# Kernel tuning notes

Measured on AMD Instinct MI355X. Metric: run time of the kernel, lower is better.

The kernel has to match this reference:

```python
import jax, jax.numpy as jnp
import numpy as np
from jax import lax


def avg_pool3(x):
    # F.avg_pool2d(x, 3, 1, 1) with count_include_pad=True: zero-pad, divide by 9.
    s = lax.reduce_window(x, 0.0, lax.add, (1, 1, 3, 3), (1, 1, 1, 1),
                          [(0, 0), (0, 0), (1, 1), (1, 1)])
    return s / 9.0


def resize_bilinear_ac(x, H, W):
    # bilinear resize with align_corners=True, separable gathers
    B, C, h, w = x.shape
    if (h, w) == (H, W):
        return x
    yc = jnp.linspace(0.0, h - 1.0, H)
    xc = jnp.linspace(0.0, w - 1.0, W)
    y0 = jnp.floor(yc).astype(jnp.int32); y1 = jnp.minimum(y0 + 1, h - 1)
    x0 = jnp.floor(xc).astype(jnp.int32); x1 = jnp.minimum(x0 + 1, w - 1)
    wy = (yc - y0).astype(x.dtype)
    wx = (xc - x0).astype(x.dtype)
    xr = x[:, :, y0, :] * (1.0 - wy)[None, None, :, None] + x[:, :, y1, :] * wy[None, None, :, None]
    return xr[:, :, :, x0] * (1.0 - wx) + xr[:, :, :, x1] * wx


def grid_sample_border(img, grid):
    # F.grid_sample(mode='bilinear', padding_mode='border', align_corners=True)
    B, C, H, W = img.shape
    x = jnp.clip((grid[..., 0] + 1.0) * 0.5 * (W - 1), 0.0, W - 1.0)
    y = jnp.clip((grid[..., 1] + 1.0) * 0.5 * (H - 1), 0.0, H - 1.0)
    x0 = jnp.floor(x).astype(jnp.int32); y0 = jnp.floor(y).astype(jnp.int32)
    x1 = jnp.minimum(x0 + 1, W - 1); y1 = jnp.minimum(y0 + 1, H - 1)
    wx = (x - x0)[..., None]; wy = (y - y0)[..., None]
    imt = jnp.transpose(img, (0, 2, 3, 1))  # [B,H,W,C]
    b = jnp.arange(B)[:, None, None]
    v00 = imt[b, y0, x0]; v01 = imt[b, y0, x1]
    v10 = imt[b, y1, x0]; v11 = imt[b, y1, x1]
    top = v00 * (1.0 - wx) + v01 * wx
    bot = v10 * (1.0 - wx) + v11 * wx
    out = top * (1.0 - wy) + bot * wy
    return jnp.transpose(out, (0, 3, 1, 2))


def warp_image(img, flow):
    B, C, H, W = img.shape
    _, _, h, w = flow.shape
    flow = resize_bilinear_ac(flow, H, W)
    scale = jnp.array([W / w, H / h], dtype=img.dtype).reshape(1, 2, 1, 1)
    flow = flow * scale
    yy, xx = jnp.meshgrid(jnp.linspace(-1.0, 1.0, H, dtype=img.dtype),
                          jnp.linspace(-1.0, 1.0, W, dtype=img.dtype), indexing='ij')
    base = jnp.stack((xx, yy), axis=-1)[None]  # [1,H,W,2]
    fn = jnp.stack([2.0 * flow[:, 0] / max(W - 1, 1),
                    2.0 * flow[:, 1] / max(H - 1, 1)], axis=-1)  # [B,H,W,2]
    return grid_sample_border(img, base + fn)


def ssim_map(x, y, C1=0.01 ** 2, C2=0.03 ** 2):
    mu_x = avg_pool3(x); mu_y = avg_pool3(y)
    sigma_x = avg_pool3(x * x) - mu_x * mu_x
    sigma_y = avg_pool3(y * y) - mu_y * mu_y
    sigma_xy = avg_pool3(x * y) - mu_x * mu_y
    ssim = (2 * mu_x * mu_y + C1) * (2 * sigma_xy + C2) / \
           ((mu_x ** 2 + mu_y ** 2 + C1) * (sigma_x + sigma_y + C2) + 1e-12)
    return jnp.mean(jnp.clip((1.0 - ssim) / 2.0, 0.0, 1.0), axis=1, keepdims=True)


def masked_mean(x, mask):
    m = (mask > 0.5).astype(x.dtype)
    num = jnp.sum(x * m)
    den = jnp.maximum(jnp.sum(m), 1.0)
    return num / den


def smoothness_loss(flow):
    dx = jnp.abs(flow[:, :, :, :-1] - flow[:, :, :, 1:])
    dy = jnp.abs(flow[:, :, :-1, :] - flow[:, :, 1:, :])
    return jnp.mean(dx) + jnp.mean(dy)


def setup_inputs() -> dict:
    key = jax.random.key(0)
    k1, k2, k3, k4 = jax.random.split(key, 4)
    B, H, W = 8, 512, 1024
    h, w = 128, 256
    return {
        'flow': jax.random.normal(k1, (B, 2, h, w), dtype=jnp.float32),
        'img1': jax.random.uniform(k2, (B, 3, H, W), dtype=jnp.float32),
        'img2': jax.random.uniform(k3, (B, 3, H, W), dtype=jnp.float32),
        'valid_mask': jax.random.uniform(k4, (B, 1, H, W), dtype=jnp.float32),
    }


def reference(flow, img1, img2, valid_mask):
    alpha_photo, alpha_smooth = 1.0, 0.1
    img2_warp = warp_image(img2, flow)
    l1 = jnp.mean(jnp.abs(img1 - img2_warp), axis=1, keepdims=True)
    photo_map = 0.85 * ssim_map(img1, img2_warp) + 0.15 * l1
    photo = masked_mean(photo_map, valid_mask)
    smooth = smoothness_loss(flow)
    total = alpha_photo * photo + alpha_smooth * smooth
    return (total, photo, smooth)
```

## Files before the change

kernel.cpp:

```cpp
#include <hip/hip_runtime.h>
#include <hip/hip_fp16.h>

#define B_   8
#define H_   512
#define W_   1024
#define FH_  128
#define FW_  256
#define TW   64
#define TH   16
#define HW_  (TW + 2)
#define HH_  (TH + 2)
#define NHALO (HH_ * HW_)
#define FR_  8
#define FC_  20
#define NSLOT 256
#define PLANE (H_ * W_)

struct alignas(8) H4 { __half2 a; __half2 b; };

__device__ __forceinline__ float wave_reduce(float v) {
    #pragma unroll
    for (int off = 32; off > 0; off >>= 1) v += __shfl_down(v, off, 64);
    return v;
}

__device__ __forceinline__ void hrow(const __half2* __restrict__ s,
                                     float& hA, float& hB, float& hAA, float& hBB, float& hAB) {
    const float2 p0 = __half22float2(s[0]);
    const float2 p1 = __half22float2(s[1]);
    const float2 p2 = __half22float2(s[2]);
    hA  = p0.x + p1.x + p2.x;
    hB  = p0.y + p1.y + p2.y;
    hAA = fmaf(p0.x, p0.x, fmaf(p1.x, p1.x, p2.x * p2.x));
    hBB = fmaf(p0.y, p0.y, fmaf(p1.y, p1.y, p2.y * p2.y));
    hAB = fmaf(p0.x, p0.y, fmaf(p1.x, p1.y, p2.x * p2.y));
}

__global__ __launch_bounds__(256)
void pack_img2(const float* __restrict__ img2, H4* __restrict__ pk) {
    const int total = B_ * PLANE;
    const int stride = gridDim.x * 256 * 4;
    for (int base = (blockIdx.x * 256 + threadIdx.x) * 4; base < total; base += stride) {
        const int b = base >> 19;
        const int p = base & (PLANE - 1);
        const float* pr = img2 + (size_t)b * 3 * PLANE;
        const float4 r  = *(const float4*)&pr[p];
        const float4 g  = *(const float4*)&pr[p + PLANE];
        const float4 bl = *(const float4*)&pr[p + 2 * PLANE];
        H4* o = pk + (size_t)b * PLANE + p;
        o[0] = { __floats2half2_rn(r.x, g.x), __floats2half2_rn(bl.x, 0.f) };
        o[1] = { __floats2half2_rn(r.y, g.y), __floats2half2_rn(bl.y, 0.f) };
        o[2] = { __floats2half2_rn(r.z, g.z), __floats2half2_rn(bl.z, 0.f) };
        o[3] = { __floats2half2_rn(r.w, g.w), __floats2half2_rn(bl.w, 0.f) };
    }
}

template <int PK>
__global__ __launch_bounds__(256, 8)
void fused_main(const float* __restrict__ flow, const float* __restrict__ img1,
                const float* __restrict__ img2, const float* __restrict__ mask,
                const H4* __restrict__ pk, float* __restrict__ accum) {
    const int bid = blockIdx.x;
    const int lin = (bid & 7) * 512 + (bid >> 3);
    const int b   = lin >> 9;
    const int rem = lin & 511;
    const int ty0 = (rem >> 4) * TH;
    const int tx0 = (rem & 15) * TW;
    const int tid = threadIdx.x;

    __shared__ __half2 sP[3][HH_][HW_];
    __shared__ float   sF[2][FR_][FC_];

    const float* f0  = flow + (size_t)b * 2 * FH_ * FW_;
    const float* f1  = f0 + FH_ * FW_;
    const float* i10 = img1 + (size_t)b * 3 * PLANE;
    const float* i11 = i10 + PLANE;
    const float* i12 = i11 + PLANE;
    const float* i20 = img2 + (size_t)b * 3 * PLANE;
    const float* i21 = i20 + PLANE;
    const float* i22 = i21 + PLANE;
    const H4*    pkb = pk + (size_t)b * PLANE;

    const int fx0s = (tx0 > 0) ? (int)((float)(tx0 - 1) * (255.0f / 1023.0f)) : 0;
    const int fy0s = (ty0 > 0) ? (int)((float)(ty0 - 1) * (127.0f / 511.0f)) : 0;
    for (int i = tid; i < 2 * FR_ * FC_; i += 256) {
        const int ch = i / (FR_ * FC_);
        const int r  = (i - ch * FR_ * FC_) / FC_;
        const int cc = i - ch * FR_ * FC_ - r * FC_;
        const int sy = min(fy0s + r, FH_ - 1);
        const int sx = min(fx0s + cc, FW_ - 1);
        const float* fp = ch ? f1 : f0;
        sF[ch][r][cc] = fp[(uint32_t)sy * FW_ + (uint32_t)sx];
    }

    const int lx  = tid & 63;
    const int lyg = tid >> 6;
    const int rb  = lyg * 4;
    const float* mb = mask + (size_t)b * PLANE;
    const uint32_t mb0 = (uint32_t)(ty0 + rb) * W_ + (uint32_t)(tx0 + lx);
    float mreg[4];
    #pragma unroll
    for (int k = 0; k < 4; ++k) mreg[k] = mb[mb0 + (uint32_t)k * W_];

    __syncthreads();

    for (int i = tid; i < NHALO; i += 256) {
        const int ly = i / HW_;
        const int lxh = i - ly * HW_;
        const int gy = ty0 + ly - 1;
        const int gx = tx0 + lxh - 1;
        float v10 = 0.f, v11 = 0.f, v12 = 0.f;
        float v20 = 0.f, v21 = 0.f, v22 = 0.f;
        if (gy >= 0 && gy < H_ && gx >= 0 && gx < W_) {
            const uint32_t p = (uint32_t)gy * W_ + (uint32_t)gx;
            v10 = i10[p]; v11 = i11[p]; v12 = i12[p];

            const float yc = gy * (127.0f / 511.0f);
            const float xc = gx * (255.0f / 1023.0f);
            const int y0 = (int)yc, x0 = (int)xc;
            const float wy = yc - (float)y0, wx = xc - (float)x0;
            const int yr = y0 - fy0s, xr = x0 - fx0s;
            const float a00 = sF[0][yr][xr],     a01 = sF[0][yr][xr + 1];
            const float a10 = sF[0][yr + 1][xr], a11 = sF[0][yr + 1][xr + 1];
            const float c00 = sF[1][yr][xr],     c01 = sF[1][yr][xr + 1];
            const float c10 = sF[1][yr + 1][xr], c11 = sF[1][yr + 1][xr + 1];
            const float fxt = fmaf(wx, a01 - a00, a00);
            const float fxb = fmaf(wx, a11 - a10, a10);
            const float fx  = fmaf(wy, fxb - fxt, fxt);
            const float fyt = fmaf(wx, c01 - c00, c00);
            const float fyb = fmaf(wx, c11 - c10, c10);
            const float fy  = fmaf(wy, fyb - fyt, fyt);

            const float gxs = fminf(fmaxf(fmaf(4.0f, fx, (float)gx), 0.0f), (float)(W_ - 1));
            const float gys = fminf(fmaxf(fmaf(4.0f, fy, (float)gy), 0.0f), (float)(H_ - 1));
            const int sx0 = (int)gxs, sy0 = (int)gys;
            const int sx1 = min(sx0 + 1, W_ - 1);
            const int sy1 = min(sy0 + 1, H_ - 1);
            const float swx = gxs - (float)sx0, swy = gys - (float)sy0;
            const uint32_t p00 = (uint32_t)sy0 * W_ + (uint32_t)sx0;
            const uint32_t p01 = (uint32_t)sy0 * W_ + (uint32_t)sx1;
            const uint32_t p10 = (uint32_t)sy1 * W_ + (uint32_t)sx0;
            const uint32_t p11 = (uint32_t)sy1 * W_ + (uint32_t)sx1;

            if (PK) {
                const H4 q00 = pkb[p00], q01 = pkb[p01], q10 = pkb[p10], q11 = pkb[p11];
                const float2 rg00 = __half22float2(q00.a), rg01 = __half22float2(q01.a);
                const float2 rg10 = __half22float2(q10.a), rg11 = __half22float2(q11.a);
                const float b00 = __low2float(q00.b), b01 = __low2float(q01.b);
                const float b10 = __low2float(q10.b), b11 = __low2float(q11.b);
                {
                    const float t = fmaf(swx, rg01.x - rg00.x, rg00.x);
                    const float u = fmaf(swx, rg11.x - rg10.x, rg10.x);
                    v20 = fmaf(swy, u - t, t);
                }
                {
                    const float t = fmaf(swx, rg01.y - rg00.y, rg00.y);
                    const float u = fmaf(swx, rg11.y - rg10.y, rg10.y);
                    v21 = fmaf(swy, u - t, t);
                }
                {
                    const float t = fmaf(swx, b01 - b00, b00);
                    const float u = fmaf(swx, b11 - b10, b10);
                    v22 = fmaf(swy, u - t, t);
                }
            } else {
                {
                    const float t = fmaf(swx, i20[p01] - i20[p00], i20[p00]);
                    const float u = fmaf(swx, i20[p11] - i20[p10], i20[p10]);
                    v20 = fmaf(swy, u - t, t);
                }
                {
                    const float t = fmaf(swx, i21[p01] - i21[p00], i21[p00]);
                    const float u = fmaf(swx, i21[p11] - i21[p10], i21[p10]);
                    v21 = fmaf(swy, u - t, t);
                }
                {
                    const float t = fmaf(swx, i22[p01] - i22[p00], i22[p00]);
                    const float u = fmaf(swx, i22[p11] - i22[p10], i22[p10]);
                    v22 = fmaf(swy, u - t, t);
                }
            }
        }
        sP[0][ly][lxh] = __floats2half2_rn(v10, v20);
        sP[1][ly][lxh] = __floats2half2_rn(v11, v21);
        sP[2][ly][lxh] = __floats2half2_rn(v12, v22);
    }

    __syncthreads();

    const float inv9 = 1.0f / 9.0f;
    const float C1 = 0.0001f, C2 = 0.0009f;
    float dist[4] = {0.f, 0.f, 0.f, 0.f};
    float l1s [4] = {0.f, 0.f, 0.f, 0.f};

    #pragma unroll
    for (int c = 0; c < 3; ++c) {
        float hA0,hB0,hAA0,hBB0,hAB0;
        float hA1,hB1,hAA1,hBB1,hAB1;
        float hA2,hB2,hAA2,hBB2,hAB2;
        hrow(&sP[c][rb + 0][lx], hA0,hB0,hAA0,hBB0,hAB0);
        hrow(&sP[c][rb + 1][lx], hA1,hB1,hAA1,hBB1,hAB1);
        #pragma unroll
        for (int k = 0; k < 4; ++k) {
            hrow(&sP[c][rb + k + 2][lx], hA2,hB2,hAA2,hBB2,hAB2);
            const float sA  = hA0  + hA1  + hA2;
            const float sB  = hB0  + hB1  + hB2;
            const float sAA = hAA0 + hAA1 + hAA2;
            const float sBB = hBB0 + hBB1 + hBB2;
            const float sAB = hAB0 + hAB1 + hAB2;
            const float mx  = sA * inv9, my = sB * inv9;
            const float vx  = fmaf(-mx, mx, sAA * inv9);
            const float vy  = fmaf(-my, my, sBB * inv9);
            const float vxy = fmaf(-mx, my, sAB * inv9);
            const float numt = (2.f * mx * my + C1) * (2.f * vxy + C2);
            const float dent = fmaf(fmaf(mx, mx, fmaf(my, my, C1)), (vx + vy + C2), 1e-12f);
            const float ssim = numt * __builtin_amdgcn_rcpf(dent);
            dist[k] += fminf(fmaxf((1.0f - ssim) * 0.5f, 0.f), 1.f);
            const float2 ctr = __half22float2(sP[c][rb + k + 1][lx + 1]);
            l1s[k] += fabsf(ctr.x - ctr.y);
            hA0 = hA1; hB0 = hB1; hAA0 = hAA1; hBB0 = hBB1; hAB0 = hAB1;
            hA1 = hA2; hB1 = hB2; hAA1 = hAA2; hBB1 = hBB2; hAB1 = hAB2;
        }
    }

    float num_acc = 0.f, den_acc = 0.f;
    #pragma unroll
    for (int k = 0; k < 4; ++k) {
        const float pmv = 0.28333334f * dist[k] + 0.05f * l1s[k];
        const float m   = (mreg[k] > 0.5f) ? 1.f : 0.f;
        num_acc = fmaf(pmv, m, num_acc);
        den_acc += m;
    }

    float num = wave_reduce(num_acc);
    float den = wave_reduce(den_acc);
    __shared__ float rn[4], rd[4];
    const int wid = tid >> 6, lane = tid & 63;
    if (lane == 0) { rn[wid] = num; rd[wid] = den; }
    __syncthreads();
    if (tid == 0) {
        float* slot = accum + (size_t)(bid & (NSLOT - 1)) * 4;
        atomicAdd(&slot[0], rn[0] + rn[1] + rn[2] + rn[3]);
        atomicAdd(&slot[1], rd[0] + rd[1] + rd[2] + rd[3]);
    }
}

__global__ __launch_bounds__(256)
void smooth_kernel(const float* __restrict__ flow, float* __restrict__ accum) {
    const int N = B_ * 2 * FH_ * FW_;
    float dxs = 0.f, dys = 0.f;
    for (int i = blockIdx.x * 256 + threadIdx.x; i < N; i += gridDim.x * 256) {
        const float f = flow[i];
        const int x = i & (FW_ - 1);
        const int y = (i >> 8) & (FH_ - 1);
        if (x < FW_ - 1) dxs += fabsf(f - flow[i + 1]);
        if (y < FH_ - 1) dys += fabsf(f - flow[i + FW_]);
    }
    dxs = wave_reduce(dxs);
    dys = wave_reduce(dys);
    __shared__ float rn[4], rd[4];
    const int wid = threadIdx.x >> 6, lane = threadIdx.x & 63;
    if (lane == 0) { rn[wid] = dxs; rd[wid] = dys; }
    __syncthreads();
    if (threadIdx.x == 0) {
        float* slot = accum + (size_t)blockIdx.x * 4;
        atomicAdd(&slot[2], rn[0] + rn[1] + rn[2] + rn[3]);
        atomicAdd(&slot[3], rd[0] + rd[1] + rd[2] + rd[3]);
    }
}

__global__ __launch_bounds__(256)
void finalize_kernel(const float* __restrict__ accum, float* __restrict__ out) {
    const int t = threadIdx.x;
    float num = accum[t * 4 + 0];
    float den = accum[t * 4 + 1];
    float dxs = accum[t * 4 + 2];
    float dys = accum[t * 4 + 3];
    num = wave_reduce(num); den = wave_reduce(den);
    dxs = wave_reduce(dxs); dys = wave_reduce(dys);
    __shared__ float r[4][4];
    const int wid = t >> 6, lane = t & 63;
    if (lane == 0) { r[wid][0] = num; r[wid][1] = den; r[wid][2] = dxs; r[wid][3] = dys; }
    __syncthreads();
    if (t == 0) {
        const float tn = r[0][0] + r[1][0] + r[2][0] + r[3][0];
        const float td = r[0][1] + r[1][1] + r[2][1] + r[3][1];
        const float tx = r[0][2] + r[1][2] + r[2][2] + r[3][2];
        const float ty = r[0][3] + r[1][3] + r[2][3] + r[3][3];
        const float photo   = tn / fmaxf(td, 1.0f);
        const float mean_dx = tx / (float)(B_ * 2 * FH_ * (FW_ - 1));
        const float mean_dy = ty / (float)(B_ * 2 * (FH_ - 1) * FW_);
        const float smooth  = mean_dx + mean_dy;
        out[0] = photo + 0.1f * smooth;
        out[1] = photo;
        out[2] = smooth;
    }
}

extern "C" void kernel_launch(void* const* d_in, const int* in_sizes, int n_in,
                              void* d_out, int out_size, void* d_ws, size_t ws_size,
                              hipStream_t stream) {
    const float* flow = (const float*)d_in[0];
    const float* img1 = (const float*)d_in[1];
    const float* img2 = (const float*)d_in[2];
    const float* mask = (const float*)d_in[3];
    float* out   = (float*)d_out;
    float* accum = (float*)d_ws;
    H4*    pk    = (H4*)((char*)d_ws + 4096);

    const size_t need = 4096 + sizeof(H4) * (size_t)B_ * PLANE;
    const bool packed = ws_size >= need;

    hipMemsetAsync(accum, 0, NSLOT * 4 * sizeof(float), stream);
    smooth_kernel<<<NSLOT, 256, 0, stream>>>(flow, accum);
    const int grid = (W_ / TW) * (H_ / TH) * B_;
    if (packed) {
        pack_img2<<<2048, 256, 0, stream>>>(img2, pk);
        fused_main<1><<<grid, 256, 0, stream>>>(flow, img1, img2, mask, pk, accum);
    } else {
        fused_main<0><<<grid, 256, 0, stream>>>(flow, img1, img2, mask, pk, accum);
    }
    finalize_kernel<<<1, 256, 0, stream>>>(accum, out);
}
```

Measured before the change: 187.9 us.

## Materialize warped img2 in separate kernel and compute SSIM window sums in packed half

Replaces the pack-to-half prepass with a kernel that computes the bilinear-warped img2 once per pixel, gathering from fp32 img2, and stores it as packed half. The main kernel then reads the precomputed warp for its halo tile, which removes the redundant warp computation on halo pixels and the shared flow staging. Separately, the 3x3 window sums, squares and cross products are computed with packed half2 arithmetic instead of fp32 to cut ALU work. This risks precision loss in variance terms and adds a full-image write/read round trip through the workspace.

```diff
diff --git a/kernel.cpp b/kernel.cpp
--- a/kernel.cpp
+++ b/kernel.cpp
@@ -24,42 +24,88 @@
     return v;
 }
 
-__device__ __forceinline__ void hrow(const __half2* __restrict__ s,
-                                     float& hA, float& hB, float& hAA, float& hBB, float& hAB) {
-    const float2 p0 = __half22float2(s[0]);
-    const float2 p1 = __half22float2(s[1]);
-    const float2 p2 = __half22float2(s[2]);
-    hA  = p0.x + p1.x + p2.x;
-    hB  = p0.y + p1.y + p2.y;
-    hAA = fmaf(p0.x, p0.x, fmaf(p1.x, p1.x, p2.x * p2.x));
-    hBB = fmaf(p0.y, p0.y, fmaf(p1.y, p1.y, p2.y * p2.y));
-    hAB = fmaf(p0.x, p0.y, fmaf(p1.x, p1.y, p2.x * p2.y));
+struct HR { __half2 s, q, c, ctr; };
+__device__ __forceinline__ HR hrowp(const __half2* __restrict__ p) {
+    const __half2 p0 = p[0], p1 = p[1], p2 = p[2];
+    HR r;
+    r.s = __hadd2(__hadd2(p0, p1), p2);
+    r.q = __hfma2(p2, p2, __hfma2(p1, p1, __hmul2(p0, p0)));
+    r.c = __hfma2(p2, __lowhigh2highlow(p2),
+          __hfma2(p1, __lowhigh2highlow(p1),
+                  __hmul2(p0, __lowhigh2highlow(p0))));
+    r.ctr = p1;
+    return r;
 }
 
 __global__ __launch_bounds__(256)
-void pack_img2(const float* __restrict__ img2, H4* __restrict__ pk) {
+void warp_img2(const float* __restrict__ flow, const float* __restrict__ img2,
+               H4* __restrict__ wp) {
     const int total = B_ * PLANE;
-    const int stride = gridDim.x * 256 * 4;
-    for (int base = (blockIdx.x * 256 + threadIdx.x) * 4; base < total; base += stride) {
-        const int b = base >> 19;
-        const int p = base & (PLANE - 1);
-        const float* pr = img2 + (size_t)b * 3 * PLANE;
-        const float4 r  = *(const float4*)&pr[p];
-        const float4 g  = *(const float4*)&pr[p + PLANE];
-        const float4 bl = *(const float4*)&pr[p + 2 * PLANE];
-        H4* o = pk + (size_t)b * PLANE + p;
-        o[0] = { __floats2half2_rn(r.x, g.x), __floats2half2_rn(bl.x, 0.f) };
-        o[1] = { __floats2half2_rn(r.y, g.y), __floats2half2_rn(bl.y, 0.f) };
-        o[2] = { __floats2half2_rn(r.z, g.z), __floats2half2_rn(bl.z, 0.f) };
-        o[3] = { __floats2half2_rn(r.w, g.w), __floats2half2_rn(bl.w, 0.f) };
-    }
-}
-
-template <int PK>
+    for (int p = blockIdx.x * 256 + threadIdx.x; p < total; p += gridDim.x * 256) {
+        const int b  = p >> 19;
+        const int pp = p & (PLANE - 1);
+        const int y  = pp >> 10;
+        const int x  = pp & (W_ - 1);
+        const float* f0  = flow + (size_t)b * 2 * FH_ * FW_;
+        const float* f1  = f0 + FH_ * FW_;
+        const float* i20 = img2 + (size_t)b * 3 * PLANE;
+        const float* i21 = i20 + PLANE;
+        const float* i22 = i21 + PLANE;
+
+        const float ycf = y * (127.0f / 511.0f);
+        const float xcf = x * (255.0f / 1023.0f);
+        const int y0 = (int)ycf, x0 = (int)xcf;
+        const int y1i = min(y0 + 1, FH_ - 1);
+        const int x1i = min(x0 + 1, FW_ - 1);
+        const float wy = ycf - (float)y0, wx = xcf - (float)x0;
+        const uint32_t r0 = (uint32_t)y0 * FW_, r1 = (uint32_t)y1i * FW_;
+        const float a00 = f0[r0 + x0], a01 = f0[r0 + x1i];
+        const float a10 = f0[r1 + x0], a11 = f0[r1 + x1i];
+        const float c00 = f1[r0 + x0], c01 = f1[r0 + x1i];
+        const float c10 = f1[r1 + x0], c11 = f1[r1 + x1i];
+        const float fxt = fmaf(wx, a01 - a00, a00);
+        const float fxb = fmaf(wx, a11 - a10, a10);
+        const float fx  = fmaf(wy, fxb - fxt, fxt);
+        const float fyt = fmaf(wx, c01 - c00, c00);
+        const float fyb = fmaf(wx, c11 - c10, c10);
+        const float fy  = fmaf(wy, fyb - fyt, fyt);
+
+        const float gxs = fminf(fmaxf(fmaf(4.0f, fx, (float)x), 0.0f), (float)(W_ - 1));
+        const float gys = fminf(fmaxf(fmaf(4.0f, fy, (float)y), 0.0f), (float)(H_ - 1));
+        const int sx0 = (int)gxs, sy0 = (int)gys;
+        const int sx1 = min(sx0 + 1, W_ - 1);
+        const int sy1 = min(sy0 + 1, H_ - 1);
+        const float swx = gxs - (float)sx0, swy = gys - (float)sy0;
+        const uint32_t p00 = (uint32_t)sy0 * W_ + (uint32_t)sx0;
+        const uint32_t p01 = (uint32_t)sy0 * W_ + (uint32_t)sx1;
+        const uint32_t p10 = (uint32_t)sy1 * W_ + (uint32_t)sx0;
+        const uint32_t p11 = (uint32_t)sy1 * W_ + (uint32_t)sx1;
+
+        float v20, v21, v22;
+        {
+            const float t = fmaf(swx, i20[p01] - i20[p00], i20[p00]);
+            const float u = fmaf(swx, i20[p11] - i20[p10], i20[p10]);
+            v20 = fmaf(swy, u - t, t);
+        }
+        {
+            const float t = fmaf(swx, i21[p01] - i21[p00], i21[p00]);
+            const float u = fmaf(swx, i21[p11] - i21[p10], i21[p10]);
+            v21 = fmaf(swy, u - t, t);
+        }
+        {
+            const float t = fmaf(swx, i22[p01] - i22[p00], i22[p00]);
+            const float u = fmaf(swx, i22[p11] - i22[p10], i22[p10]);
+            v22 = fmaf(swy, u - t, t);
+        }
+        wp[p] = { __floats2half2_rn(v20, v21), __floats2half2_rn(v22, 0.f) };
+    }
+}
+
+template <int MODE>
 __global__ __launch_bounds__(256, 8)
 void fused_main(const float* __restrict__ flow, const float* __restrict__ img1,
                 const float* __restrict__ img2, const float* __restrict__ mask,
-                const H4* __restrict__ pk, float* __restrict__ accum) {
+                const H4* __restrict__ wp, float* __restrict__ accum) {
     const int bid = blockIdx.x;
     const int lin = (bid & 7) * 512 + (bid >> 3);
     const int b   = lin >> 9;
@@ -69,29 +115,10 @@
     const int tid = threadIdx.x;
 
     __shared__ __half2 sP[3][HH_][HW_];
-    __shared__ float   sF[2][FR_][FC_];
-
-    const float* f0  = flow + (size_t)b * 2 * FH_ * FW_;
-    const float* f1  = f0 + FH_ * FW_;
+
     const float* i10 = img1 + (size_t)b * 3 * PLANE;
     const float* i11 = i10 + PLANE;
     const float* i12 = i11 + PLANE;
-    const float* i20 = img2 + (size_t)b * 3 * PLANE;
-    const float* i21 = i20 + PLANE;
-    const float* i22 = i21 + PLANE;
-    const H4*    pkb = pk + (size_t)b * PLANE;
-
-    const int fx0s = (tx0 > 0) ? (int)((float)(tx0 - 1) * (255.0f / 1023.0f)) : 0;
-    const int fy0s = (ty0 > 0) ? (int)((float)(ty0 - 1) * (127.0f / 511.0f)) : 0;
-    for (int i = tid; i < 2 * FR_ * FC_; i += 256) {
-        const int ch = i / (FR_ * FC_);
-        const int r  = (i - ch * FR_ * FC_) / FC_;
-        const int cc = i - ch * FR_ * FC_ - r * FC_;
-        const int sy = min(fy0s + r, FH_ - 1);
-        const int sx = min(fx0s + cc, FW_ - 1);
-        const float* fp = ch ? f1 : f0;
-        sF[ch][r][cc] = fp[(uint32_t)sy * FW_ + (uint32_t)sx];
-    }
 
     const int lx  = tid & 63;
     const int lyg = tid >> 6;
@@ -102,68 +129,83 @@
     #pragma unroll
     for (int k = 0; k < 4; ++k) mreg[k] = mb[mb0 + (uint32_t)k * W_];
 
-    __syncthreads();
-
-    for (int i = tid; i < NHALO; i += 256) {
-        const int ly = i / HW_;
-        const int lxh = i - ly * HW_;
-        const int gy = ty0 + ly - 1;
-        const int gx = tx0 + lxh - 1;
-        float v10 = 0.f, v11 = 0.f, v12 = 0.f;
-        float v20 = 0.f, v21 = 0.f, v22 = 0.f;
-        if (gy >= 0 && gy < H_ && gx >= 0 && gx < W_) {
-            const uint32_t p = (uint32_t)gy * W_ + (uint32_t)gx;
-            v10 = i10[p]; v11 = i11[p]; v12 = i12[p];
-
-            const float yc = gy * (127.0f / 511.0f);
-            const float xc = gx * (255.0f / 1023.0f);
-            const int y0 = (int)yc, x0 = (int)xc;
-            const float wy = yc - (float)y0, wx = xc - (float)x0;
-            const int yr = y0 - fy0s, xr = x0 - fx0s;
-            const float a00 = sF[0][yr][xr],     a01 = sF[0][yr][xr + 1];
-            const float a10 = sF[0][yr + 1][xr], a11 = sF[0][yr + 1][xr + 1];
-            const float c00 = sF[1][yr][xr],     c01 = sF[1][yr][xr + 1];
-            const float c10 = sF[1][yr + 1][xr], c11 = sF[1][yr + 1][xr + 1];
-            const float fxt = fmaf(wx, a01 - a00, a00);
-            const float fxb = fmaf(wx, a11 - a10, a10);
-            const float fx  = fmaf(wy, fxb - fxt, fxt);
-            const float fyt = fmaf(wx, c01 - c00, c00);
-            const float fyb = fmaf(wx, c11 - c10, c10);
-            const float fy  = fmaf(wy, fyb - fyt, fyt);
-
-            const float gxs = fminf(fmaxf(fmaf(4.0f, fx, (float)gx), 0.0f), (float)(W_ - 1));
-            const float gys = fminf(fmaxf(fmaf(4.0f, fy, (float)gy), 0.0f), (float)(H_ - 1));
-            const int sx0 = (int)gxs, sy0 = (int)gys;
-            const int sx1 = min(sx0 + 1, W_ - 1);
-            const int sy1 = min(sy0 + 1, H_ - 1);
-            const float swx = gxs - (float)sx0, swy = gys - (float)sy0;
-            const uint32_t p00 = (uint32_t)sy0 * W_ + (uint32_t)sx0;
-            const uint32_t p01 = (uint32_t)sy0 * W_ + (uint32_t)sx1;
-            const uint32_t p10 = (uint32_t)sy1 * W_ + (uint32_t)sx0;
-            const uint32_t p11 = (uint32_t)sy1 * W_ + (uint32_t)sx1;
-
-            if (PK) {
-                const H4 q00 = pkb[p00], q01 = pkb[p01], q10 = pkb[p10], q11 = pkb[p11];
-                const float2 rg00 = __half22float2(q00.a), rg01 = __half22float2(q01.a);
-                const float2 rg10 = __half22float2(q10.a), rg11 = __half22float2(q11.a);
-                const float b00 = __low2float(q00.b), b01 = __low2float(q01.b);
-                const float b10 = __low2float(q10.b), b11 = __low2float(q11.b);
-                {
-                    const float t = fmaf(swx, rg01.x - rg00.x, rg00.x);
-                    const float u = fmaf(swx, rg11.x - rg10.x, rg10.x);
-                    v20 = fmaf(swy, u - t, t);
-                }
-                {
-                    const float t = fmaf(swx, rg01.y - rg00.y, rg00.y);
-                    const float u = fmaf(swx, rg11.y - rg10.y, rg10.y);
-                    v21 = fmaf(swy, u - t, t);
-                }
-                {
-                    const float t = fmaf(swx, b01 - b00, b00);
-                    const float u = fmaf(swx, b11 - b10, b10);
-                    v22 = fmaf(swy, u - t, t);
-                }
+    if (MODE == 1) {
+        const H4* wpb = wp + (size_t)b * PLANE;
+        for (int i = tid; i < NHALO; i += 256) {
+            const int ly = i / HW_;
+            const int lxh = i - ly * HW_;
+            const int gy = ty0 + ly - 1;
+            const int gx = tx0 + lxh - 1;
+            __half2 o0, o1, o2;
+            if (gy >= 0 && gy < H_ && gx >= 0 && gx < W_) {
+                const uint32_t p = (uint32_t)gy * W_ + (uint32_t)gx;
+                const float v10 = i10[p], v11 = i11[p], v12 = i12[p];
+                const H4 w = wpb[p];
+                o0 = __halves2half2(__float2half_rn(v10), __low2half(w.a));
+                o1 = __halves2half2(__float2half_rn(v11), __high2half(w.a));
+                o2 = __halves2half2(__float2half_rn(v12), __low2half(w.b));
             } else {
+                o0 = __halves2half2(__float2half_rn(0.f), __float2half_rn(0.f));
+                o1 = o0; o2 = o0;
+            }
+            sP[0][ly][lxh] = o0;
+            sP[1][ly][lxh] = o1;
+            sP[2][ly][lxh] = o2;
+        }
+    } else {
+        __shared__ float sF[2][FR_][FC_];
+        const float* f0  = flow + (size_t)b * 2 * FH_ * FW_;
+        const float* f1  = f0 + FH_ * FW_;
+        const float* i20 = img2 + (size_t)b * 3 * PLANE;
+        const float* i21 = i20 + PLANE;
+        const float* i22 = i21 + PLANE;
+        const int fx0s = (tx0 > 0) ? (int)((float)(tx0 - 1) * (255.0f / 1023.0f)) : 0;
+        const int fy0s = (ty0 > 0) ? (int)((float)(ty0 - 1) * (127.0f / 511.0f)) : 0;
+        for (int i = tid; i < 2 * FR_ * FC_; i += 256) {
+            const int ch = i / (FR_ * FC_);
+            const int r  = (i - ch * FR_ * FC_) / FC_;
+            const int cc = i - ch * FR_ * FC_ - r * FC_;
+            const int sy = min(fy0s + r, FH_ - 1);
+            const int sx = min(fx0s + cc, FW_ - 1);
+            const float* fp = ch ? f1 : f0;
+            sF[ch][r][cc] = fp[(uint32_t)sy * FW_ + (uint32_t)sx];
+        }
+        __syncthreads();
+        for (int i = tid; i < NHALO; i += 256) {
+            const int ly = i / HW_;
+            const int lxh = i - ly * HW_;
+            const int gy = ty0 + ly - 1;
+            const int gx = tx0 + lxh - 1;
+            float v10 = 0.f, v11 = 0.f, v12 = 0.f;
+            float v20 = 0.f, v21 = 0.f, v22 = 0.f;
+            if (gy >= 0 && gy < H_ && gx >= 0 && gx < W_) {
+                const uint32_t p = (uint32_t)gy * W_ + (uint32_t)gx;
+                v10 = i10[p]; v11 = i11[p]; v12 = i12[p];
+                const float yc = gy * (127.0f / 511.0f);
+                const float xc = gx * (255.0f / 1023.0f);
+                const int y0 = (int)yc, x0 = (int)xc;
+                const float wy = yc - (float)y0, wx = xc - (float)x0;
+                const int yr = y0 - fy0s, xr = x0 - fx0s;
+                const float a00 = sF[0][yr][xr],     a01 = sF[0][yr][xr + 1];
+                const float a10 = sF[0][yr + 1][xr], a11 = sF[0][yr + 1][xr + 1];
+                const float c00 = sF[1][yr][xr],     c01 = sF[1][yr][xr + 1];
+                const float c10 = sF[1][yr + 1][xr], c11 = sF[1][yr + 1][xr + 1];
+                const float fxt = fmaf(wx, a01 - a00, a00);
+                const float fxb = fmaf(wx, a11 - a10, a10);
+                const float fx  = fmaf(wy, fxb - fxt, fxt);
+                const float fyt = fmaf(wx, c01 - c00, c00);
+                const float fyb = fmaf(wx, c11 - c10, c10);
+                const float fy  = fmaf(wy, fyb - fyt, fyt);
+                const float gxs = fminf(fmaxf(fmaf(4.0f, fx, (float)gx), 0.0f), (float)(W_ - 1));
+                const float gys = fminf(fmaxf(fmaf(4.0f, fy, (float)gy), 0.0f), (float)(H_ - 1));
+                const int sx0 = (int)gxs, sy0 = (int)gys;
+                const int sx1 = min(sx0 + 1, W_ - 1);
+                const int sy1 = min(sy0 + 1, H_ - 1);
+                const float swx = gxs - (float)sx0, swy = gys - (float)sy0;
+                const uint32_t p00 = (uint32_t)sy0 * W_ + (uint32_t)sx0;
+                const uint32_t p01 = (uint32_t)sy0 * W_ + (uint32_t)sx1;
+                const uint32_t p10 = (uint32_t)sy1 * W_ + (uint32_t)sx0;
+                const uint32_t p11 = (uint32_t)sy1 * W_ + (uint32_t)sx1;
                 {
                     const float t = fmaf(swx, i20[p01] - i20[p00], i20[p00]);
                     const float u = fmaf(swx, i20[p11] - i20[p10], i20[p10]);
@@ -180,10 +222,10 @@
                     v22 = fmaf(swy, u - t, t);
                 }
             }
-        }
-        sP[0][ly][lxh] = __floats2half2_rn(v10, v20);
-        sP[1][ly][lxh] = __floats2half2_rn(v11, v21);
-        sP[2][ly][lxh] = __floats2half2_rn(v12, v22);
+            sP[0][ly][lxh] = __floats2half2_rn(v10, v20);
+            sP[1][ly][lxh] = __floats2half2_rn(v11, v21);
+            sP[2][ly][lxh] = __floats2half2_rn(v12, v22);
+        }
     }
 
     __syncthreads();
@@ -195,31 +237,28 @@
 
     #pragma unroll
     for (int c = 0; c < 3; ++c) {
-        float hA0,hB0,hAA0,hBB0,hAB0;
-        float hA1,hB1,hAA1,hBB1,hAB1;
-        float hA2,hB2,hAA2,hBB2,hAB2;
-        hrow(&sP[c][rb + 0][lx], hA0,hB0,hAA0,hBB0,hAB0);
-        hrow(&sP[c][rb + 1][lx], hA1,hB1,hAA1,hBB1,hAB1);
+        HR h0 = hrowp(&sP[c][rb + 0][lx]);
+        HR h1 = hrowp(&sP[c][rb + 1][lx]);
         #pragma unroll
         for (int k = 0; k < 4; ++k) {
-            hrow(&sP[c][rb + k + 2][lx], hA2,hB2,hAA2,hBB2,hAB2);
-            const float sA  = hA0  + hA1  + hA2;
-            const float sB  = hB0  + hB1  + hB2;
-            const float sAA = hAA0 + hAA1 + hAA2;
-            const float sBB = hBB0 + hBB1 + hBB2;
-            const float sAB = hAB0 + hAB1 + hAB2;
-            const float mx  = sA * inv9, my = sB * inv9;
-            const float vx  = fmaf(-mx, mx, sAA * inv9);
-            const float vy  = fmaf(-my, my, sBB * inv9);
+            const HR h2 = hrowp(&sP[c][rb + k + 2][lx]);
+            const __half2 S = __hadd2(__hadd2(h0.s, h1.s), h2.s);
+            const __half2 Q = __hadd2(__hadd2(h0.q, h1.q), h2.q);
+            const __half2 C = __hadd2(__hadd2(h0.c, h1.c), h2.c);
+            const float2 Sf = __half22float2(S);
+            const float2 Qf = __half22float2(Q);
+            const float sAB = __low2float(C);
+            const float mx  = Sf.x * inv9, my = Sf.y * inv9;
+            const float vx  = fmaf(-mx, mx, Qf.x * inv9);
+            const float vy  = fmaf(-my, my, Qf.y * inv9);
             const float vxy = fmaf(-mx, my, sAB * inv9);
             const float numt = (2.f * mx * my + C1) * (2.f * vxy + C2);
             const float dent = fmaf(fmaf(mx, mx, fmaf(my, my, C1)), (vx + vy + C2), 1e-12f);
             const float ssim = numt * __builtin_amdgcn_rcpf(dent);
             dist[k] += fminf(fmaxf((1.0f - ssim) * 0.5f, 0.f), 1.f);
-            const float2 ctr = __half22float2(sP[c][rb + k + 1][lx + 1]);
+            const float2 ctr = __half22float2(h1.ctr);
             l1s[k] += fabsf(ctr.x - ctr.y);
-            hA0 = hA1; hB0 = hB1; hAA0 = hAA1; hBB0 = hBB1; hAB0 = hAB1;
-            hA1 = hA2; hB1 = hB2; hAA1 = hAA2; hBB1 = hBB2; hAB1 = hAB2;
+            h0 = h1; h1 = h2;
         }
     }
 
@@ -306,19 +345,19 @@
     const float* mask = (const float*)d_in[3];
     float* out   = (float*)d_out;
     float* accum = (float*)d_ws;
-    H4*    pk    = (H4*)((char*)d_ws + 4096);
+    H4*    wp    = (H4*)((char*)d_ws + 4096);
 
     const size_t need = 4096 + sizeof(H4) * (size_t)B_ * PLANE;
-    const bool packed = ws_size >= need;
+    const bool mat = ws_size >= need;
 
     hipMemsetAsync(accum, 0, NSLOT * 4 * sizeof(float), stream);
     smooth_kernel<<<NSLOT, 256, 0, stream>>>(flow, accum);
     const int grid = (W_ / TW) * (H_ / TH) * B_;
-    if (packed) {
-        pack_img2<<<2048, 256, 0, stream>>>(img2, pk);
-        fused_main<1><<<grid, 256, 0, stream>>>(flow, img1, img2, mask, pk, accum);
+    if (mat) {
+        warp_img2<<<4096, 256, 0, stream>>>(flow, img2, wp);
+        fused_main<1><<<grid, 256, 0, stream>>>(flow, img1, img2, mask, wp, accum);
     } else {
-        fused_main<0><<<grid, 256, 0, stream>>>(flow, img1, img2, mask, pk, accum);
+        fused_main<0><<<grid, 256, 0, stream>>>(flow, img1, img2, mask, wp, accum);
     }
     finalize_kernel<<<1, 256, 0, stream>>>(accum, out);
 }
```

Result: slower. 213.4 us (+13.6%).
